# Kernel optimization log

Measured on AMD Instinct MI355X. Metric: run time of the kernel, lower is better.

The kernel has to match this reference:

```python
import jax, jax.numpy as jnp
import numpy as np

TWO_PI = 6.283185307179586


def setup_inputs() -> dict:
    key = jax.random.key(0)
    k1, k2, k3, k4, k5, k6 = jax.random.split(key, 6)
    B, T, D = 2, 8192, 1024
    x = jax.random.normal(k1, (B, T, D), dtype=jnp.float32)
    # nn.Linear weights are [out, in]; init with small scale like torch default
    s = 1.0 / np.sqrt(D)
    Wk = jax.random.uniform(k2, (D, D), jnp.float32, -s, s)
    Wv = jax.random.uniform(k3, (D, D), jnp.float32, -s, s)
    Wo = jax.random.uniform(k4, (D, D), jnp.float32, -s, s)
    # random phasor frequencies in [0, 2*pi)
    freqs = jax.random.uniform(k5, (D,), jnp.float32, 0.0, TWO_PI)
    return {"x": x, "Wk": Wk, "Wv": Wv, "Wo": Wo, "freqs": freqs}


def reference(x, Wk, Wv, Wo, freqs):
    B, T, C = x.shape
    # k projection is computed in the original forward but never used downstream
    k_real = x @ Wk.T  # [B,T,D] (dead value, kept for fidelity)
    v_real = x @ Wv.T  # [B,T,D]
    v = v_real.astype(jnp.complex64)
    # rotors: per-position unit phasors exp(i * t * freqs), shape [T, D]
    t = jnp.arange(T, dtype=jnp.float32)
    rotors = jnp.exp(1j * (t[:, None] * freqs[None, :])).astype(jnp.complex64)
    # bind each value with its rotor and accumulate causally (O(N) memory trace)
    memory_trace = jnp.cumsum(v * rotors[None, :, :], axis=1)  # [B,T,D] complex64
    # retrieve by unbinding with the conjugate rotor; take the real component
    retrieved = jnp.real(memory_trace * jnp.conj(rotors)[None, :, :])  # [B,T,D]
    return retrieved @ Wo.T
```

## Files before the change

### kernel.cpp

```cpp
#include <hip/hip_runtime.h>
#include <hip/hip_bf16.h>


#define B_  2
#define T_  8192
#define D_  1024
#define BT_ 16384
#define CS_ 64
#define NCHUNK_ 128

typedef __attribute__((ext_vector_type(4))) float f32x4;
typedef __attribute__((ext_vector_type(8))) short bf16x8;

static __device__ inline unsigned short f2bf(float f) {
    union { float f; unsigned int u; } a;
    a.f = f;
    unsigned int u = a.u;
    return (unsigned short)((u + 0x7FFFu + ((u >> 16) & 1u)) >> 16);
}
static __device__ inline float bf2f(unsigned short h) {
    union { unsigned int u; float f; } a;
    a.u = ((unsigned int)h) << 16;
    return a.f;
}

__global__ __launch_bounds__(256) void cast_all(const float* __restrict__ x,
                                                const float* __restrict__ Wv,
                                                const float* __restrict__ Wo,
                                                unsigned short* __restrict__ xb,
                                                unsigned short* __restrict__ wvb,
                                                unsigned short* __restrict__ wob) {
    const int nx = BT_ * D_ / 4;
    const int nw = D_ * D_ / 4;
    int i = blockIdx.x * 256 + threadIdx.x;
    const float4* src;
    unsigned short* dst;
    int j;
    if (i < nx)            { src = (const float4*)x;  dst = xb;  j = i; }
    else if (i < nx + nw)  { src = (const float4*)Wv; dst = wvb; j = i - nx; }
    else                   { src = (const float4*)Wo; dst = wob; j = i - nx - nw; }
    float4 v = src[j];
    ushort4 o;
    o.x = f2bf(v.x); o.y = f2bf(v.y); o.z = f2bf(v.z); o.w = f2bf(v.w);
    ((ushort4*)dst)[j] = o;
}

template <bool BF16OUT, bool FUSE_SUMS>
__global__ __launch_bounds__(512, 2) void gemm_bt(const short* __restrict__ A,
                                                  const short* __restrict__ Bm,
                                                  void* __restrict__ Cout,
                                                  const float* __restrict__ freqs,
                                                  float* __restrict__ csum,
                                                  int M, int N, int K) {
    __shared__ short lds[65536];
    const int tid = threadIdx.x;
    const int lane = tid & 63;
    const int wave = tid >> 6;
    const int wm = wave >> 2, wn = wave & 3;

    const int nb = N >> 8;
    const int id = blockIdx.x;
    const int xcd = id & 7;
    const int slot = id >> 3;
    const int bn = (slot % nb) * 256;
    const int bm = (xcd * ((M >> 8) >> 3) + slot / nb) * 256;

    const int srow = lane >> 3;
    const int sg = lane & 7;
    const size_t cstep = (size_t)64 * K;
    const short* gA = A + (size_t)(bm + wave * 8 + srow) * K + ((sg ^ srow) * 8);
    const short* gB = Bm + (size_t)(bn + wave * 8 + srow) * K + ((sg ^ srow) * 8);

    auto stage1 = [&](int kt, int g) {
        const int c = g & 3;
        const short* src = ((g & 4) ? gB : gA) + c * cstep + kt * 64;
        short* dst = &lds[(kt & 1) * 32768 + ((g & 4) ? 16384 : 0) + c * 4096 + wave * 512];
        __builtin_amdgcn_global_load_lds(
            (const __attribute__((address_space(1))) void*)src,
            (__attribute__((address_space(3))) void*)dst, 16, 0, 0);
    };

    const int l15 = lane & 15;
    const int c4r = lane >> 4;
    const int swz0 = ((c4r) ^ (lane & 7)) * 8;
    const int swz1 = ((4 + c4r) ^ (lane & 7)) * 8;
    const int abase = (wm * 128 + l15) * 64;
    const int bbase = 16384 + (wn * 64 + l15) * 64;

    f32x4 acc[8][4] = {};

    stage1(0, 0); stage1(0, 1); stage1(0, 2); stage1(0, 3);
    stage1(0, 4); stage1(0, 5); stage1(0, 6); stage1(0, 7);
    stage1(1, 0); stage1(1, 2);
    stage1(1, 4); stage1(1, 5); stage1(1, 6); stage1(1, 7);
    asm volatile("s_waitcnt vmcnt(6)" ::: "memory");
    __builtin_amdgcn_sched_barrier(0);
    __builtin_amdgcn_s_barrier();

    const int NT = K >> 6;
#pragma unroll 1
    for (int t = 0; t < NT; ++t) {
        const int sb = (t & 1) * 32768;
        bf16x8 av[4][2], b01[2][2], b23[2][2];

#pragma unroll
        for (int ii = 0; ii < 4; ++ii) {
            av[ii][0] = *(const bf16x8*)&lds[sb + abase + ii * 1024 + swz0];
            av[ii][1] = *(const bf16x8*)&lds[sb + abase + ii * 1024 + swz1];
        }
#pragma unroll
        for (int j = 0; j < 2; ++j) {
            b01[j][0] = *(const bf16x8*)&lds[sb + bbase + j * 1024 + swz0];
            b01[j][1] = *(const bf16x8*)&lds[sb + bbase + j * 1024 + swz1];
        }
        if (t + 1 < NT) { stage1(t + 1, 1); stage1(t + 1, 3); }
        __builtin_amdgcn_s_barrier();
        asm volatile("s_waitcnt lgkmcnt(0)" ::: "memory");
        __builtin_amdgcn_sched_barrier(0);
        __builtin_amdgcn_s_setprio(1);
#pragma unroll
        for (int ks = 0; ks < 2; ++ks)
#pragma unroll
            for (int ii = 0; ii < 4; ++ii)
#pragma unroll
                for (int j = 0; j < 2; ++j)
                    acc[ii][j] = __builtin_amdgcn_mfma_f32_16x16x32_bf16(
                        av[ii][ks], b01[j][ks], acc[ii][j], 0, 0, 0);
        __builtin_amdgcn_s_setprio(0);
        __builtin_amdgcn_s_barrier();

#pragma unroll
        for (int j = 0; j < 2; ++j) {
            b23[j][0] = *(const bf16x8*)&lds[sb + bbase + (2 + j) * 1024 + swz0];
            b23[j][1] = *(const bf16x8*)&lds[sb + bbase + (2 + j) * 1024 + swz1];
        }
        if (t + 2 < NT) { stage1(t + 2, 0); stage1(t + 2, 2); }
        __builtin_amdgcn_s_barrier();
        asm volatile("s_waitcnt lgkmcnt(0)" ::: "memory");
        __builtin_amdgcn_sched_barrier(0);
        __builtin_amdgcn_s_setprio(1);
#pragma unroll
        for (int ks = 0; ks < 2; ++ks)
#pragma unroll
            for (int ii = 0; ii < 4; ++ii)
#pragma unroll
                for (int j = 0; j < 2; ++j)
                    acc[ii][2 + j] = __builtin_amdgcn_mfma_f32_16x16x32_bf16(
                        av[ii][ks], b23[j][ks], acc[ii][2 + j], 0, 0, 0);
        __builtin_amdgcn_s_setprio(0);
        __builtin_amdgcn_s_barrier();

#pragma unroll
        for (int ii = 0; ii < 4; ++ii) {
            av[ii][0] = *(const bf16x8*)&lds[sb + abase + (4 + ii) * 1024 + swz0];
            av[ii][1] = *(const bf16x8*)&lds[sb + abase + (4 + ii) * 1024 + swz1];
        }
        if (t + 2 < NT) { stage1(t + 2, 4); stage1(t + 2, 5); }
        __builtin_amdgcn_s_barrier();
        asm volatile("s_waitcnt lgkmcnt(0)" ::: "memory");
        __builtin_amdgcn_sched_barrier(0);
        __builtin_amdgcn_s_setprio(1);
#pragma unroll
        for (int ks = 0; ks < 2; ++ks)
#pragma unroll
            for (int ii = 0; ii < 4; ++ii)
#pragma unroll
                for (int j = 0; j < 2; ++j)
                    acc[4 + ii][2 + j] = __builtin_amdgcn_mfma_f32_16x16x32_bf16(
                        av[ii][ks], b23[j][ks], acc[4 + ii][2 + j], 0, 0, 0);
        __builtin_amdgcn_s_setprio(0);
        __builtin_amdgcn_s_barrier();

        if (t + 2 < NT) { stage1(t + 2, 6); stage1(t + 2, 7); }
        if (t + 2 < NT) asm volatile("s_waitcnt vmcnt(6)" ::: "memory");
        else            asm volatile("s_waitcnt vmcnt(0)" ::: "memory");
        __builtin_amdgcn_sched_barrier(0);
        __builtin_amdgcn_s_barrier();
        __builtin_amdgcn_s_setprio(1);
#pragma unroll
        for (int ks = 0; ks < 2; ++ks)
#pragma unroll
            for (int ii = 0; ii < 4; ++ii)
#pragma unroll
                for (int j = 0; j < 2; ++j)
                    acc[4 + ii][j] = __builtin_amdgcn_mfma_f32_16x16x32_bf16(
                        av[ii][ks], b01[j][ks], acc[4 + ii][j], 0, 0, 0);
        __builtin_amdgcn_s_setprio(0);
        __builtin_amdgcn_s_barrier();
    }

    const int row0 = c4r * 4;
#pragma unroll
    for (int i = 0; i < 8; ++i) {
#pragma unroll
        for (int j = 0; j < 4; ++j) {
            const int col = bn + wn * 64 + j * 16 + (lane & 15);
#pragma unroll
            for (int r = 0; r < 4; ++r) {
                const size_t row = (size_t)bm + wm * 128 + i * 16 + row0 + r;
                if constexpr (BF16OUT)
                    ((unsigned short*)Cout)[row * N + col] = f2bf(acc[i][j][r]);
                else
                    ((float*)Cout)[row * N + col] = acc[i][j][r];
            }
        }
    }

    if constexpr (FUSE_SUMS) {
        const int b = bm >> 13;
        const int trow = bm & 8191;
#pragma unroll
        for (int ig = 0; ig < 2; ++ig) {
            const int chunk = (trow >> 6) + wm * 2 + ig;
            const int t0 = trow + wm * 128 + ig * 64 + c4r * 4;
#pragma unroll
            for (int j = 0; j < 4; ++j) {
                const int d = bn + wn * 64 + j * 16 + (lane & 15);
                const float f = freqs[d];
                float ss, cc2;
                sincosf((float)t0 * f, &ss, &cc2);
                float s1, c1;
                sincosf(f, &s1, &c1);
                float c2 = c1 * c1 - s1 * s1, s2 = 2.f * c1 * s1;
                float c4 = c2 * c2 - s2 * s2, s4 = 2.f * c2 * s2;
                float c8 = c4 * c4 - s4 * s4, s8 = 2.f * c4 * s4;
                float c12 = c8 * c4 - s8 * s4, s12 = s8 * c4 + c8 * s4;
                float c13 = c12 * c1 - s12 * s1, s13 = s12 * c1 + c12 * s1;
                float ar = 0.f, ai = 0.f;
                float cr = cc2, sr2 = ss;
#pragma unroll
                for (int ii = 0; ii < 4; ++ii) {
                    const int i = ig * 4 + ii;
#pragma unroll
                    for (int r = 0; r < 4; ++r) {
                        const float w = acc[i][j][r];
                        ar = fmaf(w, cr, ar); ai = fmaf(w, sr2, ai);
                        const float ec = (r < 3) ? c1 : c13;
                        const float es = (r < 3) ? s1 : s13;
                        const float nc = cr * ec - sr2 * es;
                        const float ns = sr2 * ec + cr * es;
                        cr = nc; sr2 = ns;
                    }
                }
                ar += __shfl_xor(ar, 16); ai += __shfl_xor(ai, 16);
                ar += __shfl_xor(ar, 32); ai += __shfl_xor(ai, 32);
                if (c4r == 0)
                    *(float2*)(csum + (((size_t)b * NCHUNK_ + chunk) * D_ + d) * 2) =
                        make_float2(ar, ai);
            }
        }
    }
}

__global__ __launch_bounds__(256) void scan_pass2(float* __restrict__ csum) {
    const int g = blockIdx.x * 256 + threadIdx.x;
    const int b = g / D_;
    const int d = g % D_;
    float2* cs = (float2*)csum;
    const size_t base = (size_t)b * NCHUNK_ * D_ + d;
    float pr = 0.f, pi = 0.f;
    for (int cc = 0; cc < NCHUNK_; cc += 32) {
        float2 buf[32];
#pragma unroll
        for (int k = 0; k < 32; ++k) buf[k] = cs[base + (size_t)(cc + k) * D_];
#pragma unroll
        for (int k = 0; k < 32; ++k) {
            float r = buf[k].x, im = buf[k].y;
            buf[k] = make_float2(pr, pi);
            pr += r; pi += im;
        }
#pragma unroll
        for (int k = 0; k < 32; ++k) cs[base + (size_t)(cc + k) * D_] = buf[k];
    }
}

__global__ __launch_bounds__(256) void scan_pass3(const unsigned short* __restrict__ v,
                                                  const float* __restrict__ freqs,
                                                  const float* __restrict__ csum,
                                                  unsigned short* __restrict__ ret) {
    const int chunk = blockIdx.x;
    const int d0 = blockIdx.y * 512 + threadIdx.x * 2;
    const int b = blockIdx.z;

    float fr[2], s[2], c[2], sf[2], cf[2], ar[2], ai[2];
    {
        float2 f2 = *(const float2*)(freqs + d0);
        fr[0] = f2.x; fr[1] = f2.y;
    }
    const float t0f = (float)(chunk * CS_);
#pragma unroll
    for (int k = 0; k < 2; ++k) {
        sincosf(t0f * fr[k], &s[k], &c[k]);
        sincosf(fr[k], &sf[k], &cf[k]);
    }
    {
        const float4 o = *(const float4*)(csum + (((size_t)b * NCHUNK_ + chunk) * D_ + d0) * 2);
        ar[0] = o.x; ai[0] = o.y; ar[1] = o.z; ai[1] = o.w;
    }
    const unsigned int* vp = (const unsigned int*)(v + ((size_t)b * T_ + chunk * CS_) * D_ + d0);
    unsigned int* rp = (unsigned int*)(ret + ((size_t)b * T_ + chunk * CS_) * D_ + d0);
    for (int tb = 0; tb < CS_; tb += 8) {
        unsigned int w[8];
#pragma unroll
        for (int u = 0; u < 8; ++u) w[u] = vp[(size_t)(tb + u) * (D_ / 2)];
#pragma unroll
        for (int u = 0; u < 8; ++u) {
            float wv[2], o[2];
            wv[0] = bf2f((unsigned short)w[u]);
            wv[1] = bf2f((unsigned short)(w[u] >> 16));
#pragma unroll
            for (int k = 0; k < 2; ++k) {
                ar[k] = fmaf(wv[k], c[k], ar[k]);
                ai[k] = fmaf(wv[k], s[k], ai[k]);
                o[k] = ar[k] * c[k] + ai[k] * s[k];
                float nc = c[k] * cf[k] - s[k] * sf[k];
                float ns = s[k] * cf[k] + c[k] * sf[k];
                c[k] = nc; s[k] = ns;
            }
            rp[(size_t)(tb + u) * (D_ / 2)] =
                (unsigned int)f2bf(o[0]) | ((unsigned int)f2bf(o[1]) << 16);
        }
    }
}

extern "C" void kernel_launch(void* const* d_in, const int* in_sizes, int n_in,
                              void* d_out, int out_size, void* d_ws, size_t ws_size,
                              hipStream_t stream) {
    const float* x     = (const float*)d_in[0];
    const float* Wv    = (const float*)d_in[2];
    const float* Wo    = (const float*)d_in[3];
    const float* freqs = (const float*)d_in[4];
    float* out = (float*)d_out;

    char* ws = (char*)d_ws;
    unsigned short* x_bf  = (unsigned short*)ws;
    unsigned short* Wv_bf = (unsigned short*)(ws + 33554432);
    unsigned short* Wo_bf = (unsigned short*)(ws + 35651584);
    unsigned short* ret   = (unsigned short*)(ws + 37748736);
    float*          csum  = (float*)(ws + 71303168);
    unsigned short* v_bf = (unsigned short*)d_out;

    cast_all<<<(BT_ * D_ / 4 + 2 * D_ * D_ / 4) / 256, 256, 0, stream>>>(
        x, Wv, Wo, x_bf, Wv_bf, Wo_bf);

    gemm_bt<true, true><<<(BT_ / 256) * (D_ / 256), 512, 0, stream>>>(
        (const short*)x_bf, (const short*)Wv_bf, (void*)v_bf, freqs, csum, BT_, D_, D_);

    scan_pass2<<<(B_ * D_) / 256, 256, 0, stream>>>(csum);
    dim3 p3grid(NCHUNK_, D_ / 512, B_);
    scan_pass3<<<p3grid, 256, 0, stream>>>(v_bf, freqs, csum, ret);

    gemm_bt<false, false><<<(BT_ / 256) * (D_ / 256), 512, 0, stream>>>(
        (const short*)ret, (const short*)Wo_bf, (void*)out, nullptr, nullptr, BT_, D_, D_);
}
```

Baseline: 235.0 us.

## Switch GEMM inner loop from 16x16x32 to 32x32x16 bf16 MFMA tiles

Replaces the 16x16x32 MFMA accumulation with 32x32x16 MFMA instructions, reorganising LDS fragment loads (four k-slices per 64-wide tile), the accumulator layout, the epilogue stores and the fused chunk-sum phasor recurrence to match the 32x32 output layout. It also reorders the prefetch schedule of the next-next tile stages and adjusts the vmcnt waits. The aim is fewer MFMA issues and LDS reads per FLOP. The cost is larger accumulator vectors and a different store pattern; the row mapping must match the 32x32 MFMA layout for correctness.

```diff
diff --git a/kernel.cpp b/kernel.cpp
--- a/kernel.cpp
+++ b/kernel.cpp
@@ -10,6 +10,7 @@
 #define NCHUNK_ 128
 
 typedef __attribute__((ext_vector_type(4))) float f32x4;
+typedef __attribute__((ext_vector_type(16))) float f32x16;
 typedef __attribute__((ext_vector_type(8))) short bf16x8;
 
 static __device__ inline unsigned short f2bf(float f) {
@@ -80,20 +81,22 @@
             (__attribute__((address_space(3))) void*)dst, 16, 0, 0);
     };
 
-    const int l15 = lane & 15;
-    const int c4r = lane >> 4;
-    const int swz0 = ((c4r) ^ (lane & 7)) * 8;
-    const int swz1 = ((4 + c4r) ^ (lane & 7)) * 8;
-    const int abase = (wm * 128 + l15) * 64;
-    const int bbase = 16384 + (wn * 64 + l15) * 64;
-
-    f32x4 acc[8][4] = {};
-
-    stage1(0, 0); stage1(0, 1); stage1(0, 2); stage1(0, 3);
-    stage1(0, 4); stage1(0, 5); stage1(0, 6); stage1(0, 7);
-    stage1(1, 0); stage1(1, 2);
-    stage1(1, 4); stage1(1, 5); stage1(1, 6); stage1(1, 7);
-    asm volatile("s_waitcnt vmcnt(6)" ::: "memory");
+    const int l31 = lane & 31;
+    const int hi = lane >> 5;
+    const int l7 = lane & 7;
+    int swz[4];
+#pragma unroll
+    for (int ks = 0; ks < 4; ++ks) swz[ks] = ((ks * 2 + hi) ^ l7) * 8;
+    const int abase = (wm * 128 + l31) * 64;
+    const int bbase = 16384 + (wn * 64 + l31) * 64;
+
+    f32x16 acc[4][2] = {};
+
+#pragma unroll
+    for (int g = 0; g < 8; ++g) stage1(0, g);
+#pragma unroll
+    for (int g = 0; g < 8; ++g) stage1(1, g);
+    asm volatile("s_waitcnt vmcnt(8)" ::: "memory");
     __builtin_amdgcn_sched_barrier(0);
     __builtin_amdgcn_s_barrier();
 
@@ -101,107 +104,95 @@
 #pragma unroll 1
     for (int t = 0; t < NT; ++t) {
         const int sb = (t & 1) * 32768;
-        bf16x8 av[4][2], b01[2][2], b23[2][2];
-
-#pragma unroll
-        for (int ii = 0; ii < 4; ++ii) {
-            av[ii][0] = *(const bf16x8*)&lds[sb + abase + ii * 1024 + swz0];
-            av[ii][1] = *(const bf16x8*)&lds[sb + abase + ii * 1024 + swz1];
-        }
-#pragma unroll
-        for (int j = 0; j < 2; ++j) {
-            b01[j][0] = *(const bf16x8*)&lds[sb + bbase + j * 1024 + swz0];
-            b01[j][1] = *(const bf16x8*)&lds[sb + bbase + j * 1024 + swz1];
-        }
-        if (t + 1 < NT) { stage1(t + 1, 1); stage1(t + 1, 3); }
+        const bool pf = (t + 2 < NT);
+        bf16x8 av[2][4], b0[4], b1[4];
+
+#pragma unroll
+        for (int ks = 0; ks < 4; ++ks) {
+            av[0][ks] = *(const bf16x8*)&lds[sb + abase + 0 * 2048 + swz[ks]];
+            av[1][ks] = *(const bf16x8*)&lds[sb + abase + 1 * 2048 + swz[ks]];
+            b0[ks]    = *(const bf16x8*)&lds[sb + bbase + 0 * 2048 + swz[ks]];
+        }
         __builtin_amdgcn_s_barrier();
         asm volatile("s_waitcnt lgkmcnt(0)" ::: "memory");
         __builtin_amdgcn_sched_barrier(0);
         __builtin_amdgcn_s_setprio(1);
 #pragma unroll
-        for (int ks = 0; ks < 2; ++ks)
-#pragma unroll
-            for (int ii = 0; ii < 4; ++ii)
-#pragma unroll
-                for (int j = 0; j < 2; ++j)
-                    acc[ii][j] = __builtin_amdgcn_mfma_f32_16x16x32_bf16(
-                        av[ii][ks], b01[j][ks], acc[ii][j], 0, 0, 0);
+        for (int ks = 0; ks < 4; ++ks)
+#pragma unroll
+            for (int f = 0; f < 2; ++f)
+                acc[f][0] = __builtin_amdgcn_mfma_f32_32x32x16_bf16(
+                    av[f][ks], b0[ks], acc[f][0], 0, 0, 0);
         __builtin_amdgcn_s_setprio(0);
         __builtin_amdgcn_s_barrier();
 
 #pragma unroll
-        for (int j = 0; j < 2; ++j) {
-            b23[j][0] = *(const bf16x8*)&lds[sb + bbase + (2 + j) * 1024 + swz0];
-            b23[j][1] = *(const bf16x8*)&lds[sb + bbase + (2 + j) * 1024 + swz1];
-        }
-        if (t + 2 < NT) { stage1(t + 2, 0); stage1(t + 2, 2); }
+        for (int ks = 0; ks < 4; ++ks)
+            b1[ks] = *(const bf16x8*)&lds[sb + bbase + 1 * 2048 + swz[ks]];
+        if (pf) { stage1(t + 2, 0); stage1(t + 2, 2); }
         __builtin_amdgcn_s_barrier();
         asm volatile("s_waitcnt lgkmcnt(0)" ::: "memory");
         __builtin_amdgcn_sched_barrier(0);
         __builtin_amdgcn_s_setprio(1);
 #pragma unroll
-        for (int ks = 0; ks < 2; ++ks)
-#pragma unroll
-            for (int ii = 0; ii < 4; ++ii)
-#pragma unroll
-                for (int j = 0; j < 2; ++j)
-                    acc[ii][2 + j] = __builtin_amdgcn_mfma_f32_16x16x32_bf16(
-                        av[ii][ks], b23[j][ks], acc[ii][2 + j], 0, 0, 0);
+        for (int ks = 0; ks < 4; ++ks)
+#pragma unroll
+            for (int f = 0; f < 2; ++f)
+                acc[f][1] = __builtin_amdgcn_mfma_f32_32x32x16_bf16(
+                    av[f][ks], b1[ks], acc[f][1], 0, 0, 0);
         __builtin_amdgcn_s_setprio(0);
         __builtin_amdgcn_s_barrier();
 
 #pragma unroll
-        for (int ii = 0; ii < 4; ++ii) {
-            av[ii][0] = *(const bf16x8*)&lds[sb + abase + (4 + ii) * 1024 + swz0];
-            av[ii][1] = *(const bf16x8*)&lds[sb + abase + (4 + ii) * 1024 + swz1];
-        }
-        if (t + 2 < NT) { stage1(t + 2, 4); stage1(t + 2, 5); }
+        for (int ks = 0; ks < 4; ++ks) {
+            av[0][ks] = *(const bf16x8*)&lds[sb + abase + 2 * 2048 + swz[ks]];
+            av[1][ks] = *(const bf16x8*)&lds[sb + abase + 3 * 2048 + swz[ks]];
+        }
+        if (pf) { stage1(t + 2, 4); stage1(t + 2, 5); stage1(t + 2, 6); stage1(t + 2, 7); }
         __builtin_amdgcn_s_barrier();
         asm volatile("s_waitcnt lgkmcnt(0)" ::: "memory");
         __builtin_amdgcn_sched_barrier(0);
         __builtin_amdgcn_s_setprio(1);
 #pragma unroll
-        for (int ks = 0; ks < 2; ++ks)
-#pragma unroll
-            for (int ii = 0; ii < 4; ++ii)
-#pragma unroll
-                for (int j = 0; j < 2; ++j)
-                    acc[4 + ii][2 + j] = __builtin_amdgcn_mfma_f32_16x16x32_bf16(
-                        av[ii][ks], b23[j][ks], acc[4 + ii][2 + j], 0, 0, 0);
+        for (int ks = 0; ks < 4; ++ks)
+#pragma unroll
+            for (int f = 0; f < 2; ++f)
+                acc[2 + f][1] = __builtin_amdgcn_mfma_f32_32x32x16_bf16(
+                    av[f][ks], b1[ks], acc[2 + f][1], 0, 0, 0);
         __builtin_amdgcn_s_setprio(0);
         __builtin_amdgcn_s_barrier();
 
-        if (t + 2 < NT) { stage1(t + 2, 6); stage1(t + 2, 7); }
-        if (t + 2 < NT) asm volatile("s_waitcnt vmcnt(6)" ::: "memory");
-        else            asm volatile("s_waitcnt vmcnt(0)" ::: "memory");
+        if (pf) { stage1(t + 2, 1); stage1(t + 2, 3); }
+        if (pf) asm volatile("s_waitcnt vmcnt(8)" ::: "memory");
+        else    asm volatile("s_waitcnt vmcnt(0)" ::: "memory");
         __builtin_amdgcn_sched_barrier(0);
         __builtin_amdgcn_s_barrier();
         __builtin_amdgcn_s_setprio(1);
 #pragma unroll
-        for (int ks = 0; ks < 2; ++ks)
-#pragma unroll
-            for (int ii = 0; ii < 4; ++ii)
-#pragma unroll
-                for (int j = 0; j < 2; ++j)
-                    acc[4 + ii][j] = __builtin_amdgcn_mfma_f32_16x16x32_bf16(
-                        av[ii][ks], b01[j][ks], acc[4 + ii][j], 0, 0, 0);
+        for (int ks = 0; ks < 4; ++ks)
+#pragma unroll
+            for (int f = 0; f < 2; ++f)
+                acc[2 + f][0] = __builtin_amdgcn_mfma_f32_32x32x16_bf16(
+                    av[f][ks], b0[ks], acc[2 + f][0], 0, 0, 0);
         __builtin_amdgcn_s_setprio(0);
         __builtin_amdgcn_s_barrier();
     }
 
-    const int row0 = c4r * 4;
-#pragma unroll
-    for (int i = 0; i < 8; ++i) {
-#pragma unroll
-        for (int j = 0; j < 4; ++j) {
-            const int col = bn + wn * 64 + j * 16 + (lane & 15);
-#pragma unroll
-            for (int r = 0; r < 4; ++r) {
-                const size_t row = (size_t)bm + wm * 128 + i * 16 + row0 + r;
-                if constexpr (BF16OUT)
-                    ((unsigned short*)Cout)[row * N + col] = f2bf(acc[i][j][r]);
-                else
-                    ((float*)Cout)[row * N + col] = acc[i][j][r];
+#pragma unroll
+    for (int fi = 0; fi < 4; ++fi) {
+#pragma unroll
+        for (int j = 0; j < 2; ++j) {
+            const int col = bn + wn * 64 + j * 32 + l31;
+#pragma unroll
+            for (int rq = 0; rq < 4; ++rq) {
+#pragma unroll
+                for (int rr = 0; rr < 4; ++rr) {
+                    const size_t row = (size_t)bm + wm * 128 + fi * 32 + rq * 8 + 4 * hi + rr;
+                    if constexpr (BF16OUT)
+                        ((unsigned short*)Cout)[row * N + col] = f2bf(acc[fi][j][rq * 4 + rr]);
+                    else
+                        ((float*)Cout)[row * N + col] = acc[fi][j][rq * 4 + rr];
+                }
             }
         }
     }
@@ -212,10 +203,10 @@
 #pragma unroll
         for (int ig = 0; ig < 2; ++ig) {
             const int chunk = (trow >> 6) + wm * 2 + ig;
-            const int t0 = trow + wm * 128 + ig * 64 + c4r * 4;
-#pragma unroll
-            for (int j = 0; j < 4; ++j) {
-                const int d = bn + wn * 64 + j * 16 + (lane & 15);
+            const int t0 = trow + wm * 128 + ig * 64 + 4 * hi;
+#pragma unroll
+            for (int j = 0; j < 2; ++j) {
+                const int d = bn + wn * 64 + j * 32 + l31;
                 const float f = freqs[d];
                 float ss, cc2;
                 sincosf((float)t0 * f, &ss, &cc2);
@@ -223,28 +214,27 @@
                 sincosf(f, &s1, &c1);
                 float c2 = c1 * c1 - s1 * s1, s2 = 2.f * c1 * s1;
                 float c4 = c2 * c2 - s2 * s2, s4 = 2.f * c2 * s2;
-                float c8 = c4 * c4 - s4 * s4, s8 = 2.f * c4 * s4;
-                float c12 = c8 * c4 - s8 * s4, s12 = s8 * c4 + c8 * s4;
-                float c13 = c12 * c1 - s12 * s1, s13 = s12 * c1 + c12 * s1;
+                float c5 = c4 * c1 - s4 * s1, s5 = s4 * c1 + c4 * s1;
                 float ar = 0.f, ai = 0.f;
                 float cr = cc2, sr2 = ss;
 #pragma unroll
-                for (int ii = 0; ii < 4; ++ii) {
-                    const int i = ig * 4 + ii;
-#pragma unroll
-                    for (int r = 0; r < 4; ++r) {
-                        const float w = acc[i][j][r];
-                        ar = fmaf(w, cr, ar); ai = fmaf(w, sr2, ai);
-                        const float ec = (r < 3) ? c1 : c13;
-                        const float es = (r < 3) ? s1 : s13;
-                        const float nc = cr * ec - sr2 * es;
-                        const float ns = sr2 * ec + cr * es;
-                        cr = nc; sr2 = ns;
+                for (int f2 = 0; f2 < 2; ++f2) {
+#pragma unroll
+                    for (int rq = 0; rq < 4; ++rq) {
+#pragma unroll
+                        for (int rr = 0; rr < 4; ++rr) {
+                            const float w = acc[ig * 2 + f2][j][rq * 4 + rr];
+                            ar = fmaf(w, cr, ar); ai = fmaf(w, sr2, ai);
+                            const float ec = (rr < 3) ? c1 : c5;
+                            const float es = (rr < 3) ? s1 : s5;
+                            const float nc = cr * ec - sr2 * es;
+                            const float ns = sr2 * ec + cr * es;
+                            cr = nc; sr2 = ns;
+                        }
                     }
                 }
-                ar += __shfl_xor(ar, 16); ai += __shfl_xor(ai, 16);
                 ar += __shfl_xor(ar, 32); ai += __shfl_xor(ai, 32);
-                if (c4r == 0)
+                if (hi == 0)
                     *(float2*)(csum + (((size_t)b * NCHUNK_ + chunk) * D_ + d) * 2) =
                         make_float2(ar, ai);
             }
```

New measurement: 246.4 us. 1.05x slower.
